# Kernel tuning notes

Measured on AMD Instinct MI355X. Metric: run time of the kernel, lower is better.

The kernel has to match this reference:

```python
import jax, jax.numpy as jnp
import numpy as np

OUT = 7        # output_size
SR = 2         # sampling_ratio
SCALE = 0.0625 # spatial_scale (stride 16)


def setup_inputs() -> dict:
    key = jax.random.key(0)
    k1, k2, k3, k4 = jax.random.split(key, 4)
    N, C, H, W, K = 4, 256, 128, 128, 1000
    x = jax.random.normal(k1, (N, C, H, W), dtype=jnp.float32)
    b = jax.random.randint(k2, (K,), 0, N).astype(jnp.float32)
    xy = jax.random.uniform(k3, (K, 2), minval=0.0, maxval=1800.0)
    wh = jax.random.uniform(k4, (K, 2), minval=16.0, maxval=248.0)
    rois = jnp.concatenate([b[:, None], xy, xy + wh], axis=1)  # [K,5]
    return {"x": x, "rois": rois}


def _roi_align(x, rois):
    # x: [N,C,H,W], rois: [K,5] = (batch_idx, x1, y1, x2, y2); aligned=False (roi_end_mode=0)
    N, C, H, W = x.shape
    K = rois.shape[0]
    G = OUT * SR  # dense sample grid per ROI (14x14)
    bidx = rois[:, 0].astype(jnp.int32)
    sx = rois[:, 1] * SCALE
    sy = rois[:, 2] * SCALE
    ex = rois[:, 3] * SCALE
    ey = rois[:, 4] * SCALE
    rw = jnp.maximum(ex - sx, 1.0)
    rh = jnp.maximum(ey - sy, 1.0)
    # sample-point centers: y = sy + bin_h*(g+0.5)/SR over flattened grid index g
    g = (jnp.arange(G, dtype=jnp.float32) + 0.5) / SR
    ys = sy[:, None] + (rh / OUT)[:, None] * g[None, :]  # [K,G]
    xs = sx[:, None] + (rw / OUT)[:, None] * g[None, :]  # [K,G]

    def corners(v, L):
        valid = (v > -1.0) & (v < L)
        vc = jnp.clip(v, 0.0, L - 1.0)
        lo = jnp.floor(vc).astype(jnp.int32)
        hi = jnp.minimum(lo + 1, L - 1)
        frac = vc - lo.astype(jnp.float32)
        return lo, hi, frac, valid

    y0, y1, fy, vy = corners(ys, H)
    x0, x1, fx, vx = corners(xs, W)
    b3 = bidx[:, None, None]

    def gather(yy, xx):
        # -> [K,G,G,C] (channel slice moves to last axis)
        return x[b3, :, yy[:, :, None], xx[:, None, :]]

    v00 = gather(y0, x0)
    v01 = gather(y0, x1)
    v10 = gather(y1, x0)
    v11 = gather(y1, x1)
    fy_ = fy[:, :, None, None]
    fx_ = fx[:, None, :, None]
    val = (v00 * (1.0 - fy_) * (1.0 - fx_) + v01 * (1.0 - fy_) * fx_
           + v10 * fy_ * (1.0 - fx_) + v11 * fy_ * fx_)
    mask = (vy[:, :, None] & vx[:, None, :])[..., None]
    val = jnp.where(mask, val, 0.0)
    # average-pool SRxSR samples per output bin
    pooled = val.reshape(K, OUT, SR, OUT, SR, C).mean(axis=(2, 4))  # [K,OUT,OUT,C]
    return jnp.transpose(pooled, (0, 3, 1, 2))  # [K,C,OUT,OUT]


def reference(x, rois):
    return _roi_align(x, rois)
```

## Files before the change

kernel.cpp:

```cpp
#include <hip/hip_runtime.h>

#define NB    4
#define CCH   256
#define HH    128
#define WW    128
#define HW    (HH * WW)
#define CHW   (CCH * HW)
#define PBINS 49
#define OUT_PER_ROI (CCH * PBINS)

__global__ __launch_bounds__(256) void xpose_nchw_nhwc(
    const float* __restrict__ src, float* __restrict__ dst) {
  __shared__ float tile[64][65];
  const int n   = blockIdx.z;
  const int hw0 = blockIdx.x * 64;
  const int c0  = blockIdx.y * 64;
  const float* s = src + (size_t)n * CHW;
  float*       d = dst + (size_t)n * CHW;
  const int tx = threadIdx.x;
  const int ty = threadIdx.y;

#pragma unroll
  for (int r = 0; r < 4; ++r) {
    const int c = ty + 16 * r;
    const float4 v =
        *(const float4*)(s + (size_t)(c0 + c) * HW + hw0 + 4 * tx);
    tile[c][4 * tx + 0] = v.x;
    tile[c][4 * tx + 1] = v.y;
    tile[c][4 * tx + 2] = v.z;
    tile[c][4 * tx + 3] = v.w;
  }
  __syncthreads();
#pragma unroll
  for (int r = 0; r < 4; ++r) {
    const int h = ty + 16 * r;
    float4 v;
    v.x = tile[4 * tx + 0][h];
    v.y = tile[4 * tx + 1][h];
    v.z = tile[4 * tx + 2][h];
    v.w = tile[4 * tx + 3][h];
    *(float4*)(d + (size_t)(hw0 + h) * CCH + c0 + 4 * tx) = v;
  }
}

__global__ __launch_bounds__(512) void roi_align_nhwc(
    const float* __restrict__ xt, const float* __restrict__ rois,
    float* __restrict__ out) {
  __shared__ float s_pool[OUT_PER_ROI];
  __shared__ float s_fy[14], s_fx[14];
  __shared__ int   s_y0[14], s_y1[14], s_x0[14], s_x1[14], s_vy[14], s_vx[14];

  const int k   = blockIdx.x;
  const int tid = threadIdx.x;
  const float* r = rois + 5 * k;
  const int   n  = (int)r[0];
  const float sx = r[1] * 0.0625f, sy = r[2] * 0.0625f;
  const float ex = r[3] * 0.0625f, ey = r[4] * 0.0625f;
  const float rw = fmaxf(ex - sx, 1.0f);
  const float rh = fmaxf(ey - sy, 1.0f);

  if (tid < 14) {
    float g  = ((float)tid + 0.5f) * 0.5f;
    float v  = sy + (rh / 7.0f) * g;
    int   ok = (v > -1.0f) && (v < 128.0f);
    float vc = fminf(fmaxf(v, 0.0f), 127.0f);
    int   lo = (int)floorf(vc);
    s_y0[tid] = lo;
    s_y1[tid] = min(lo + 1, 127);
    s_fy[tid] = vc - (float)lo;
    s_vy[tid] = ok;
  } else if (tid >= 64 && tid < 78) {
    int   j  = tid - 64;
    float g  = ((float)j + 0.5f) * 0.5f;
    float v  = sx + (rw / 7.0f) * g;
    int   ok = (v > -1.0f) && (v < 128.0f);
    float vc = fminf(fmaxf(v, 0.0f), 127.0f);
    int   lo = (int)floorf(vc);
    s_x0[j] = lo;
    s_x1[j] = min(lo + 1, 127);
    s_fx[j] = vc - (float)lo;
    s_vx[j] = ok;
  }
  __syncthreads();

  const int wv   = tid >> 6;
  const int lane = tid & 63;
  const float* xbase = xt + ((size_t)n << 22) + (lane << 2);

  for (int p = wv; p < PBINS; p += 8) {
    const int ph = p / 7;
    const int pw = p - 7 * ph;
    float a0 = 0.f, a1 = 0.f, a2 = 0.f, a3 = 0.f;
#pragma unroll
    for (int iy = 0; iy < 2; ++iy) {
      const int   gy = 2 * ph + iy;
      const int   vy = s_vy[gy];
      const float fy = s_fy[gy];
      const int   y0 = s_y0[gy], y1 = s_y1[gy];
#pragma unroll
      for (int ix = 0; ix < 2; ++ix) {
        const int gx = 2 * pw + ix;
        if (vy && s_vx[gx]) {
          const float fx = s_fx[gx];
          const int   x0 = s_x0[gx], x1 = s_x1[gx];
          const float4 v00 = *(const float4*)(xbase + (y0 << 15) + (x0 << 8));
          const float4 v01 = *(const float4*)(xbase + (y0 << 15) + (x1 << 8));
          const float4 v10 = *(const float4*)(xbase + (y1 << 15) + (x0 << 8));
          const float4 v11 = *(const float4*)(xbase + (y1 << 15) + (x1 << 8));
          const float w00 = (1.f - fy) * (1.f - fx);
          const float w01 = (1.f - fy) * fx;
          const float w10 = fy * (1.f - fx);
          const float w11 = fy * fx;
          a0 += w00 * v00.x + w01 * v01.x + w10 * v10.x + w11 * v11.x;
          a1 += w00 * v00.y + w01 * v01.y + w10 * v10.y + w11 * v11.y;
          a2 += w00 * v00.z + w01 * v01.z + w10 * v10.z + w11 * v11.z;
          a3 += w00 * v00.w + w01 * v01.w + w10 * v10.w + w11 * v11.w;
        }
      }
    }
    const int cb = lane << 2;
    s_pool[(cb + 0) * PBINS + p] = a0 * 0.25f;
    s_pool[(cb + 1) * PBINS + p] = a1 * 0.25f;
    s_pool[(cb + 2) * PBINS + p] = a2 * 0.25f;
    s_pool[(cb + 3) * PBINS + p] = a3 * 0.25f;
  }
  __syncthreads();

  float* o = out + (size_t)k * OUT_PER_ROI;
  for (int i = tid; i < OUT_PER_ROI; i += 512) o[i] = s_pool[i];
}

__global__ __launch_bounds__(256) void roi_align_nchw(
    const float* __restrict__ x, const float* __restrict__ rois,
    float* __restrict__ out, int total) {
  int idx = blockIdx.x * 256 + threadIdx.x;
  if (idx >= total) return;
  int k  = idx / OUT_PER_ROI;
  int rr = idx - k * OUT_PER_ROI;
  int c  = rr / PBINS;
  int p  = rr - c * PBINS;
  int ph = p / 7, pw = p - 7 * ph;
  const float* r = rois + 5 * k;
  int   n  = (int)r[0];
  float sx = r[1] * 0.0625f, sy = r[2] * 0.0625f;
  float ex = r[3] * 0.0625f, ey = r[4] * 0.0625f;
  float rw = fmaxf(ex - sx, 1.0f);
  float rh = fmaxf(ey - sy, 1.0f);
  const float* xb = x + ((size_t)n * CCH + c) * HW;
  float acc = 0.f;
  for (int iy = 0; iy < 2; ++iy) {
    float g  = (float)(2 * ph + iy) + 0.5f;
    float v  = sy + (rh / 7.0f) * (g * 0.5f);
    if (!(v > -1.0f && v < 128.0f)) continue;
    float vc = fminf(fmaxf(v, 0.0f), 127.0f);
    int   y0 = (int)floorf(vc);
    int   y1 = min(y0 + 1, 127);
    float fy = vc - (float)y0;
    for (int ix = 0; ix < 2; ++ix) {
      float gx  = (float)(2 * pw + ix) + 0.5f;
      float vx_ = sx + (rw / 7.0f) * (gx * 0.5f);
      if (!(vx_ > -1.0f && vx_ < 128.0f)) continue;
      float vcx = fminf(fmaxf(vx_, 0.0f), 127.0f);
      int   x0  = (int)floorf(vcx);
      int   x1  = min(x0 + 1, 127);
      float fx  = vcx - (float)x0;
      float v00 = xb[y0 * WW + x0], v01 = xb[y0 * WW + x1];
      float v10 = xb[y1 * WW + x0], v11 = xb[y1 * WW + x1];
      acc += v00 * (1.f - fy) * (1.f - fx) + v01 * (1.f - fy) * fx +
             v10 * fy * (1.f - fx) + v11 * fy * fx;
    }
  }
  out[idx] = acc * 0.25f;
}

extern "C" void kernel_launch(void* const* d_in, const int* in_sizes, int n_in,
                              void* d_out, int out_size, void* d_ws, size_t ws_size,
                              hipStream_t stream) {
  const float* x    = (const float*)d_in[0];
  const float* rois = (const float*)d_in[1];
  float*       out  = (float*)d_out;
  const int K = in_sizes[1] / 5;

  const size_t need = (size_t)NB * CHW * sizeof(float);
  if (ws_size >= need) {
    float* xt = (float*)d_ws;
    dim3 tb(16, 16, 1);
    dim3 tg(HW / 64, CCH / 64, NB);
    xpose_nchw_nhwc<<<tg, tb, 0, stream>>>(x, xt);
    roi_align_nhwc<<<K, 512, 0, stream>>>(xt, rois, out);
  } else {
    const int total = K * OUT_PER_ROI;
    roi_align_nchw<<<(total + 255) / 256, 256, 0, stream>>>(x, rois, out, total);
  }
}
```

Measured before the change: 149.8 us.

## Store transposed NHWC feature map in bf16 and branch-free bilinear gather

The transpose kernel now writes the NHWC copy of the input as bf16 (round-to-nearest-even), halving the workspace write and the gather read traffic. The ROI kernel reads bf16 and widens it to fp32, folds the validity masks into precomputed weights to remove branches, precomputes row and column offsets, processes two bins per loop iteration, and writes its output with float4 stores. The bf16 storage introduces rounding error in the inputs, which may exceed the accuracy tolerance.

```diff
diff --git a/kernel.cpp b/kernel.cpp
--- a/kernel.cpp
+++ b/kernel.cpp
@@ -9,46 +9,94 @@
 #define PBINS 49
 #define OUT_PER_ROI (CCH * PBINS)
 
-__global__ __launch_bounds__(256) void xpose_nchw_nhwc(
-    const float* __restrict__ src, float* __restrict__ dst) {
+typedef __attribute__((ext_vector_type(8))) unsigned short ushort8_t;
+
+__device__ __forceinline__ unsigned short f2bf(float f) {
+  unsigned u = __float_as_uint(f);
+  unsigned r = u + 0x7fffu + ((u >> 16) & 1u);
+  return (unsigned short)(r >> 16);
+}
+
+__device__ __forceinline__ float4 ld4bf(const unsigned short* p) {
+  ushort4 v = *(const ushort4*)p;
+  return make_float4(__uint_as_float((unsigned)v.x << 16),
+                     __uint_as_float((unsigned)v.y << 16),
+                     __uint_as_float((unsigned)v.z << 16),
+                     __uint_as_float((unsigned)v.w << 16));
+}
+
+__global__ __launch_bounds__(256) void xpose_nchw_nhwc_bf16(
+    const float* __restrict__ src, unsigned short* __restrict__ dst) {
   __shared__ float tile[64][65];
   const int n   = blockIdx.z;
   const int hw0 = blockIdx.x * 64;
   const int c0  = blockIdx.y * 64;
   const float* s = src + (size_t)n * CHW;
-  float*       d = dst + (size_t)n * CHW;
-  const int tx = threadIdx.x;
-  const int ty = threadIdx.y;
+  unsigned short* d = dst + (size_t)n * CHW;
+  const int tid = threadIdx.x;
+  const int tx = tid & 15, ty = tid >> 4;
 
 #pragma unroll
   for (int r = 0; r < 4; ++r) {
     const int c = ty + 16 * r;
-    const float4 v =
-        *(const float4*)(s + (size_t)(c0 + c) * HW + hw0 + 4 * tx);
+    const float4 v = *(const float4*)(s + (size_t)(c0 + c) * HW + hw0 + 4 * tx);
     tile[c][4 * tx + 0] = v.x;
     tile[c][4 * tx + 1] = v.y;
     tile[c][4 * tx + 2] = v.z;
     tile[c][4 * tx + 3] = v.w;
   }
   __syncthreads();
-#pragma unroll
-  for (int r = 0; r < 4; ++r) {
-    const int h = ty + 16 * r;
-    float4 v;
-    v.x = tile[4 * tx + 0][h];
-    v.y = tile[4 * tx + 1][h];
-    v.z = tile[4 * tx + 2][h];
-    v.w = tile[4 * tx + 3][h];
-    *(float4*)(d + (size_t)(hw0 + h) * CCH + c0 + 4 * tx) = v;
-  }
-}
-
-__global__ __launch_bounds__(512) void roi_align_nhwc(
-    const float* __restrict__ xt, const float* __restrict__ rois,
+
+  const int row = tid >> 3;
+  const int cg  = tid & 7;
+#pragma unroll
+  for (int r = 0; r < 2; ++r) {
+    const int h = row + 32 * r;
+    ushort8_t o;
+#pragma unroll
+    for (int j = 0; j < 8; ++j) o[j] = f2bf(tile[cg * 8 + j][h]);
+    *(ushort8_t*)(d + (size_t)(hw0 + h) * CCH + c0 + cg * 8) = o;
+  }
+}
+
+__device__ __forceinline__ float4 bin_compute(
+    const unsigned short* __restrict__ xbase, int p,
+    const float* __restrict__ wy0, const float* __restrict__ wy1,
+    const float* __restrict__ wx0, const float* __restrict__ wx1,
+    const int (*__restrict__ oy)[2], const int (*__restrict__ ox)[2]) {
+  const int ph = p / 7, pw = p - 7 * ph;
+  float4 a = make_float4(0.f, 0.f, 0.f, 0.f);
+#pragma unroll
+  for (int iy = 0; iy < 2; ++iy) {
+    const int   gy  = 2 * ph + iy;
+    const float wyA = wy0[gy], wyB = wy1[gy];
+    const int   oyA = oy[gy][0], oyB = oy[gy][1];
+#pragma unroll
+    for (int ix = 0; ix < 2; ++ix) {
+      const int   gx  = 2 * pw + ix;
+      const float wxA = wx0[gx], wxB = wx1[gx];
+      const int   oxA = ox[gx][0], oxB = ox[gx][1];
+      const float4 c00 = ld4bf(xbase + oyA + oxA);
+      const float4 c01 = ld4bf(xbase + oyA + oxB);
+      const float4 c10 = ld4bf(xbase + oyB + oxA);
+      const float4 c11 = ld4bf(xbase + oyB + oxB);
+      const float w00 = wyA * wxA, w01 = wyA * wxB;
+      const float w10 = wyB * wxA, w11 = wyB * wxB;
+      a.x += w00 * c00.x + w01 * c01.x + w10 * c10.x + w11 * c11.x;
+      a.y += w00 * c00.y + w01 * c01.y + w10 * c10.y + w11 * c11.y;
+      a.z += w00 * c00.z + w01 * c01.z + w10 * c10.z + w11 * c11.z;
+      a.w += w00 * c00.w + w01 * c01.w + w10 * c10.w + w11 * c11.w;
+    }
+  }
+  return a;
+}
+
+__global__ __launch_bounds__(512, 6) void roi_align_nhwc_bf16(
+    const unsigned short* __restrict__ xt, const float* __restrict__ rois,
     float* __restrict__ out) {
   __shared__ float s_pool[OUT_PER_ROI];
-  __shared__ float s_fy[14], s_fx[14];
-  __shared__ int   s_y0[14], s_y1[14], s_x0[14], s_x1[14], s_vy[14], s_vx[14];
+  __shared__ float s_wy0[14], s_wy1[14], s_wx0[14], s_wx1[14];
+  __shared__ int   s_oy[14][2], s_ox[14][2];
 
   const int k   = blockIdx.x;
   const int tid = threadIdx.x;
@@ -62,72 +110,56 @@
   if (tid < 14) {
     float g  = ((float)tid + 0.5f) * 0.5f;
     float v  = sy + (rh / 7.0f) * g;
-    int   ok = (v > -1.0f) && (v < 128.0f);
+    float m  = ((v > -1.0f) && (v < 128.0f)) ? 1.0f : 0.0f;
     float vc = fminf(fmaxf(v, 0.0f), 127.0f);
     int   lo = (int)floorf(vc);
-    s_y0[tid] = lo;
-    s_y1[tid] = min(lo + 1, 127);
-    s_fy[tid] = vc - (float)lo;
-    s_vy[tid] = ok;
+    float fy = vc - (float)lo;
+    s_wy0[tid] = (1.0f - fy) * m;
+    s_wy1[tid] = fy * m;
+    s_oy[tid][0] = lo << 15;
+    s_oy[tid][1] = min(lo + 1, 127) << 15;
   } else if (tid >= 64 && tid < 78) {
     int   j  = tid - 64;
     float g  = ((float)j + 0.5f) * 0.5f;
     float v  = sx + (rw / 7.0f) * g;
-    int   ok = (v > -1.0f) && (v < 128.0f);
+    float m  = ((v > -1.0f) && (v < 128.0f)) ? 1.0f : 0.0f;
     float vc = fminf(fmaxf(v, 0.0f), 127.0f);
     int   lo = (int)floorf(vc);
-    s_x0[j] = lo;
-    s_x1[j] = min(lo + 1, 127);
-    s_fx[j] = vc - (float)lo;
-    s_vx[j] = ok;
+    float fx = vc - (float)lo;
+    s_wx0[j] = (1.0f - fx) * m;
+    s_wx1[j] = fx * m;
+    s_ox[j][0] = lo << 8;
+    s_ox[j][1] = min(lo + 1, 127) << 8;
   }
   __syncthreads();
 
   const int wv   = tid >> 6;
   const int lane = tid & 63;
-  const float* xbase = xt + ((size_t)n << 22) + (lane << 2);
-
-  for (int p = wv; p < PBINS; p += 8) {
-    const int ph = p / 7;
-    const int pw = p - 7 * ph;
-    float a0 = 0.f, a1 = 0.f, a2 = 0.f, a3 = 0.f;
-#pragma unroll
-    for (int iy = 0; iy < 2; ++iy) {
-      const int   gy = 2 * ph + iy;
-      const int   vy = s_vy[gy];
-      const float fy = s_fy[gy];
-      const int   y0 = s_y0[gy], y1 = s_y1[gy];
-#pragma unroll
-      for (int ix = 0; ix < 2; ++ix) {
-        const int gx = 2 * pw + ix;
-        if (vy && s_vx[gx]) {
-          const float fx = s_fx[gx];
-          const int   x0 = s_x0[gx], x1 = s_x1[gx];
-          const float4 v00 = *(const float4*)(xbase + (y0 << 15) + (x0 << 8));
-          const float4 v01 = *(const float4*)(xbase + (y0 << 15) + (x1 << 8));
-          const float4 v10 = *(const float4*)(xbase + (y1 << 15) + (x0 << 8));
-          const float4 v11 = *(const float4*)(xbase + (y1 << 15) + (x1 << 8));
-          const float w00 = (1.f - fy) * (1.f - fx);
-          const float w01 = (1.f - fy) * fx;
-          const float w10 = fy * (1.f - fx);
-          const float w11 = fy * fx;
-          a0 += w00 * v00.x + w01 * v01.x + w10 * v10.x + w11 * v11.x;
-          a1 += w00 * v00.y + w01 * v01.y + w10 * v10.y + w11 * v11.y;
-          a2 += w00 * v00.z + w01 * v01.z + w10 * v10.z + w11 * v11.z;
-          a3 += w00 * v00.w + w01 * v01.w + w10 * v10.w + w11 * v11.w;
-        }
-      }
+  const unsigned short* xbase = xt + ((size_t)n << 22) + (lane << 2);
+  const int cb = lane << 2;
+
+  for (int p0 = wv; p0 < PBINS; p0 += 16) {
+    const int p1 = p0 + 8;
+    float4 a0 = bin_compute(xbase, p0, s_wy0, s_wy1, s_wx0, s_wx1, s_oy, s_ox);
+    float4 a1 = make_float4(0.f, 0.f, 0.f, 0.f);
+    if (p1 < PBINS)
+      a1 = bin_compute(xbase, p1, s_wy0, s_wy1, s_wx0, s_wx1, s_oy, s_ox);
+    s_pool[(cb + 0) * PBINS + p0] = a0.x * 0.25f;
+    s_pool[(cb + 1) * PBINS + p0] = a0.y * 0.25f;
+    s_pool[(cb + 2) * PBINS + p0] = a0.z * 0.25f;
+    s_pool[(cb + 3) * PBINS + p0] = a0.w * 0.25f;
+    if (p1 < PBINS) {
+      s_pool[(cb + 0) * PBINS + p1] = a1.x * 0.25f;
+      s_pool[(cb + 1) * PBINS + p1] = a1.y * 0.25f;
+      s_pool[(cb + 2) * PBINS + p1] = a1.z * 0.25f;
+      s_pool[(cb + 3) * PBINS + p1] = a1.w * 0.25f;
     }
-    const int cb = lane << 2;
-    s_pool[(cb + 0) * PBINS + p] = a0 * 0.25f;
-    s_pool[(cb + 1) * PBINS + p] = a1 * 0.25f;
-    s_pool[(cb + 2) * PBINS + p] = a2 * 0.25f;
-    s_pool[(cb + 3) * PBINS + p] = a3 * 0.25f;
   }
   __syncthreads();
 
-  float* o = out + (size_t)k * OUT_PER_ROI;
-  for (int i = tid; i < OUT_PER_ROI; i += 512) o[i] = s_pool[i];
+  float4*       op = (float4*)(out + (size_t)k * OUT_PER_ROI);
+  const float4* sp = (const float4*)s_pool;
+  for (int i = tid; i < OUT_PER_ROI / 4; i += 512) op[i] = sp[i];
 }
 
 __global__ __launch_bounds__(256) void roi_align_nchw(
@@ -181,13 +213,13 @@
   float*       out  = (float*)d_out;
   const int K = in_sizes[1] / 5;
 
-  const size_t need = (size_t)NB * CHW * sizeof(float);
+  const size_t need = (size_t)NB * CHW * sizeof(unsigned short);
   if (ws_size >= need) {
-    float* xt = (float*)d_ws;
-    dim3 tb(16, 16, 1);
+    unsigned short* xt = (unsigned short*)d_ws;
+    dim3 tb(256, 1, 1);
     dim3 tg(HW / 64, CCH / 64, NB);
-    xpose_nchw_nhwc<<<tg, tb, 0, stream>>>(x, xt);
-    roi_align_nhwc<<<K, 512, 0, stream>>>(xt, rois, out);
+    xpose_nchw_nhwc_bf16<<<tg, tb, 0, stream>>>(x, xt);
+    roi_align_nhwc_bf16<<<K, 512, 0, stream>>>(xt, rois, out);
   } else {
     const int total = K * OUT_PER_ROI;
     roi_align_nchw<<<(total + 255) / 256, 256, 0, stream>>>(x, rois, out, total);
```

Measured after the change: 178.6 us. 1.19x slower.
